# Kernel optimization log

Hardware: AMD Instinct MI355X
Metric: run time of the kernel (lower is better)

## Reference

```python
import jax, jax.numpy as jnp
import numpy as np

N = 100_000   # nodes
E = 1_600_000 # edges (avg degree 16)
IN_DIM = 128
OUT_DIM = 64
NEG_SLOPE = 0.2  # PyG GATConv default


def setup_inputs() -> dict:
    key = jax.random.key(0)
    k_x, k_ei, k_w, k_as, k_ad = jax.random.split(key, 5)
    x = jax.random.normal(k_x, (N, IN_DIM), dtype=jnp.float32)
    edge_index = jax.random.randint(k_ei, (2, E), 0, N, dtype=jnp.int32)
    # GATConv params (heads=1): linear weight, attention vectors, output bias
    W = jax.random.normal(k_w, (IN_DIM, OUT_DIM), dtype=jnp.float32) / np.sqrt(IN_DIM)
    a_src = jax.random.normal(k_as, (OUT_DIM,), dtype=jnp.float32) * 0.1
    a_dst = jax.random.normal(k_ad, (OUT_DIM,), dtype=jnp.float32) * 0.1
    bias = jnp.zeros((OUT_DIM,), dtype=jnp.float32)
    return {"x": x, "edge_index": edge_index, "W": W, "a_src": a_src, "a_dst": a_dst, "bias": bias}


def reference(x, edge_index, W, a_src, a_dst, bias):
    # PyG GATConv, heads=1, add_self_loops=True
    h = x @ W                                   # [N, OUT]
    loop = jnp.arange(N, dtype=edge_index.dtype)
    ei = jnp.concatenate([edge_index, jnp.stack([loop, loop])], axis=1)  # [2, E+N]
    src, dst = ei[0], ei[1]
    # per-node attention logits, gathered per edge
    alpha_s = h @ a_src                         # [N]
    alpha_d = h @ a_dst                         # [N]
    e = alpha_s[src] + alpha_d[dst]             # [E+N]
    e = jnp.where(e > 0, e, NEG_SLOPE * e)      # leaky_relu
    # segment softmax over edges sharing the same destination node
    m = jax.ops.segment_max(e, dst, num_segments=N)   # every node has a self loop
    ex = jnp.exp(e - m[dst])
    s = jax.ops.segment_sum(ex, dst, num_segments=N)
    alpha = ex / s[dst]                         # [E+N]
    # weighted scatter-add of source messages
    out = jax.ops.segment_sum(alpha[:, None] * h[src], dst, num_segments=N)  # [N, OUT]
    return out + bias
```

## Files before the change

### kernel.cpp

```cpp
#include <hip/hip_runtime.h>
#include <hip/hip_bf16.h>

#ifndef NEG_SLOPE
#define NEG_SLOPE 0.2f
#endif

#define GRP_SHIFT 9
#define GRP_SIZE 512
#define NGMAX 256
#define MS_CHUNK 4096
#define BKT_CAP 10240

typedef short bf16x8 __attribute__((ext_vector_type(8)));
typedef float f32x4 __attribute__((ext_vector_type(4)));

__device__ __forceinline__ unsigned short f2bf(float f) {
    union { float f; unsigned int u; } c; c.f = f;
    unsigned int r = (c.u + 0x7FFFu + ((c.u >> 16) & 1u)) >> 16;
    return (unsigned short)r;
}
__device__ __forceinline__ float bf2f(unsigned short u) {
    union { unsigned int u; float f; } c; c.u = ((unsigned int)u) << 16;
    return c.f;
}
__device__ __forceinline__ float bflo(unsigned int u) {
    union { unsigned int u; float f; } c; c.u = u << 16;
    return c.f;
}
__device__ __forceinline__ float bfhi(unsigned int u) {
    union { unsigned int u; float f; } c; c.u = u & 0xffff0000u;
    return c.f;
}

struct GemmSmem {
    unsigned short xb[64 * 136];
    unsigned short wt[64 * 136];
};
struct MsSmem {
    unsigned int pack[MS_CHUNK];
    unsigned char gtag[MS_CHUNK];
    int hist[NGMAX];
    int gb[NGMAX];
    int wsum[4];
};
union FusedSmem {
    GemmSmem g;
    MsSmem m;
};

__global__ __launch_bounds__(256) void gemm_ms_kernel(
    const float* __restrict__ x, const float* __restrict__ W,
    const float* __restrict__ a_src, const float* __restrict__ a_dst,
    unsigned short* __restrict__ hb, float* __restrict__ as_,
    float* __restrict__ ad_, const int* __restrict__ ei,
    int* __restrict__ cursor, unsigned int* __restrict__ pairs,
    int N, int E, int NG, int nchunk)
{
    __shared__ FusedSmem sm;
    const int tid = threadIdx.x;

    if ((int)blockIdx.x < nchunk) {
        unsigned int* ls_pack = sm.m.pack;
        unsigned char* ls_g = sm.m.gtag;
        int* ls_hist = sm.m.hist;
        int* ls_gb = sm.m.gb;
        int* ls_wsum = sm.m.wsum;

        const int cs = (int)blockIdx.x * MS_CHUNK;
        const int n = min(MS_CHUNK, E - cs);
        const int* srcp = ei + cs;
        const int* dstp = ei + E + cs;

        ls_hist[tid] = 0;
        __syncthreads();
        for (int i = tid; i < n; i += 256)
            atomicAdd(&ls_hist[dstp[i] >> GRP_SHIFT], 1);
        __syncthreads();

        const int h = ls_hist[tid];
        const int lane = tid & 63;
        int incl = h;
#pragma unroll
        for (int off = 1; off < 64; off <<= 1) {
            const int t = __shfl_up(incl, off);
            if (lane >= off) incl += t;
        }
        const int wv = tid >> 6;
        if (lane == 63) ls_wsum[wv] = incl;
        __syncthreads();
        int wpre = 0;
        for (int w = 0; w < wv; ++w) wpre += ls_wsum[w];
        const int excl = wpre + incl - h;
        if (tid < NG && h > 0) {
            const int old = atomicAdd(&cursor[tid], h);
            ls_gb[tid] = tid * BKT_CAP + old - excl;
        }
        __syncthreads();
        ls_hist[tid] = excl;
        __syncthreads();

        for (int i = tid; i < n; i += 256) {
            const int src = srcp[i];
            const int dst = dstp[i];
            const int g = dst >> GRP_SHIFT;
            const int idx = atomicAdd(&ls_hist[g], 1);
            ls_pack[idx] = ((unsigned int)src << GRP_SHIFT) | (unsigned int)(dst & (GRP_SIZE - 1));
            ls_g[idx] = (unsigned char)g;
        }
        __syncthreads();

        for (int i = tid; i < n; i += 256) {
            const int g = ls_g[i];
            const int pos = ls_gb[g] + i;
            if (pos < (g + 1) * BKT_CAP)
                pairs[pos] = ls_pack[i];
        }
    } else {
        unsigned short* xb = sm.g.xb;
        unsigned short* wt = sm.g.wt;
        const int r0 = ((int)blockIdx.x - nchunk) * 64;

        for (int idx = tid; idx < 2048; idx += 256) {
            const int r = idx >> 5;
            const int c4 = idx & 31;
            const int row = r0 + r;
            float4 v = make_float4(0.f, 0.f, 0.f, 0.f);
            if (row < N) v = ((const float4*)(x + (size_t)row * 128))[c4];
            ushort4 o;
            o.x = f2bf(v.x); o.y = f2bf(v.y); o.z = f2bf(v.z); o.w = f2bf(v.w);
            *(ushort4*)(xb + r * 136 + c4 * 4) = o;
        }
        {
            const int n = tid & 63;
            const int kb = (tid >> 6) * 32;
            for (int kk = 0; kk < 32; ++kk) {
                const int k = kb + kk;
                wt[n * 136 + k] = f2bf(W[k * 64 + n]);
            }
        }
        __syncthreads();

        const int wv = tid >> 6;
        const int lane = tid & 63;
        const int m16 = lane & 15;
        const int quad = lane >> 4;

        f32x4 acc[4];
#pragma unroll
        for (int ct = 0; ct < 4; ++ct) acc[ct] = (f32x4){0.f, 0.f, 0.f, 0.f};

        const unsigned short* xrow = xb + (wv * 16 + m16) * 136;
#pragma unroll
        for (int kq = 0; kq < 4; ++kq) {
            const int k0 = kq * 32;
            const bf16x8 a = *(const bf16x8*)(xrow + k0 + quad * 8);
#pragma unroll
            for (int ct = 0; ct < 4; ++ct) {
                const bf16x8 b = *(const bf16x8*)(wt + (ct * 16 + m16) * 136 + k0 + quad * 8);
                acc[ct] = __builtin_amdgcn_mfma_f32_16x16x32_bf16(a, b, acc[ct], 0, 0, 0);
            }
        }

#pragma unroll
        for (int ct = 0; ct < 4; ++ct) {
#pragma unroll
            for (int rg = 0; rg < 4; ++rg) {
                const int row = r0 + wv * 16 + quad * 4 + rg;
                if (row < N) hb[(size_t)row * 64 + ct * 16 + m16] = f2bf(acc[ct][rg]);
            }
        }

        float asv[4], adv[4];
#pragma unroll
        for (int ct = 0; ct < 4; ++ct) {
            asv[ct] = a_src[ct * 16 + m16];
            adv[ct] = a_dst[ct * 16 + m16];
        }
#pragma unroll
        for (int rg = 0; rg < 4; ++rg) {
            float ps = acc[0][rg] * asv[0] + acc[1][rg] * asv[1] +
                       acc[2][rg] * asv[2] + acc[3][rg] * asv[3];
            float pd = acc[0][rg] * adv[0] + acc[1][rg] * adv[1] +
                       acc[2][rg] * adv[2] + acc[3][rg] * adv[3];
#pragma unroll
            for (int off = 1; off < 16; off <<= 1) {
                ps += __shfl_xor(ps, off);
                pd += __shfl_xor(pd, off);
            }
            const int row = r0 + wv * 16 + quad * 4 + rg;
            if (m16 == 0 && row < N) { as_[row] = ps; ad_[row] = pd; }
        }
    }
}

__global__ __launch_bounds__(1024) void group_sort_kernel(
    const unsigned int* __restrict__ pairs, const int* __restrict__ cursor,
    unsigned int* __restrict__ meta, int* __restrict__ csr, int N)
{
    __shared__ int sdeg[GRP_SIZE];
    __shared__ int scur[GRP_SIZE];
    __shared__ int swsum[8];
    __shared__ int ssrc[BKT_CAP];
    const int g = blockIdx.x;
    const int tid = threadIdx.x;
    const int eb0 = g * BKT_CAP;
    const int cnt = min(cursor[g], BKT_CAP);

    if (tid < GRP_SIZE) sdeg[tid] = 0;
    __syncthreads();
    for (int i = tid; i < cnt; i += 1024)
        atomicAdd(&sdeg[pairs[eb0 + i] & (GRP_SIZE - 1)], 1);
    __syncthreads();

    int s = 0, incl = 0;
    if (tid < GRP_SIZE) {
        s = sdeg[tid];
        const int lane = tid & 63;
        incl = s;
#pragma unroll
        for (int off = 1; off < 64; off <<= 1) {
            const int t = __shfl_up(incl, off);
            if (lane >= off) incl += t;
        }
        if (lane == 63) swsum[tid >> 6] = incl;
    }
    __syncthreads();
    if (tid < GRP_SIZE) {
        int wpre = 0;
        const int wv = tid >> 6;
        for (int w = 0; w < wv; ++w) wpre += swsum[w];
        const int excl = wpre + incl - s;
        scur[tid] = excl;
        const int node = (g << GRP_SHIFT) + tid;
        if (node < N)
            meta[node] = ((unsigned int)(eb0 + excl) << 10) | (unsigned int)min(s, 1023);
    }
    __syncthreads();

    for (int i = tid; i < cnt; i += 1024) {
        const unsigned int p = pairs[eb0 + i];
        const int idx = atomicAdd(&scur[p & (GRP_SIZE - 1)], 1);
        ssrc[idx] = (int)(p >> GRP_SHIFT);
    }
    __syncthreads();
    for (int i = tid; i < cnt; i += 1024)
        csr[eb0 + i] = ssrc[i];
}

__device__ void aggregate_slow(
    const unsigned short* __restrict__ h, const float* __restrict__ as_,
    const float* __restrict__ ad_, const int* __restrict__ csr,
    const float* __restrict__ bias, float* __restrict__ out,
    int wid, int p0, int deg, int lane)
{
    const float adi = ad_[wid];
    float e0 = as_[wid] + adi;
    e0 = e0 > 0.f ? e0 : NEG_SLOPE * e0;
    float m = e0, ll = 1.f;
    float acc = bf2f(h[(size_t)wid * 64 + lane]);
    const int p1 = p0 + deg;
    for (int p = p0; p < p1; ++p) {
        const int sj = csr[p];
        float ee = as_[sj] + adi;
        ee = ee > 0.f ? ee : NEG_SLOPE * ee;
        const float nm = fmaxf(m, ee);
        const float sc = __expf(m - nm);
        const float pp = __expf(ee - nm);
        ll = ll * sc + pp;
        acc = acc * sc + pp * bf2f(h[(size_t)sj * 64 + lane]);
        m = nm;
    }
    out[(size_t)wid * 64 + lane] = acc / ll + bias[lane];
}

__global__ __launch_bounds__(256) void aggregate_kernel(
    const unsigned short* __restrict__ h, const float* __restrict__ as_,
    const float* __restrict__ ad_, const unsigned int* __restrict__ meta,
    const int* __restrict__ csr, const float* __restrict__ bias,
    float* __restrict__ out, int N)
{
    const int wbase = (blockIdx.x * 256 + threadIdx.x) >> 6;
    const int lane = threadIdx.x & 63;
    const int widA = wbase * 2;
    if (widA >= N) return;
    const int widB = widA + 1;
    const bool hasB = (widB < N);

    const unsigned int mtA = meta[widA];
    const unsigned int mtB = hasB ? meta[widB] : 0u;
    const int p0A = (int)(mtA >> 10), degA = (int)(mtA & 1023u);
    const int p0B = (int)(mtB >> 10), degB = (int)(mtB & 1023u);

    if (degA <= 63 && degB <= 63) {
        const float adiA = ad_[widA];
        const float adiB = hasB ? ad_[widB] : 0.f;
        float e0A = as_[widA] + adiA;
        e0A = e0A > 0.f ? e0A : NEG_SLOPE * e0A;
        float e0B = hasB ? as_[widB] + adiB : 0.f;
        e0B = e0B > 0.f ? e0B : NEG_SLOPE * e0B;

        int sA = widA, sB = hasB ? widB : widA;
        float eA = -1e30f, eB = -1e30f;
        if (lane < degA) {
            sA = csr[p0A + lane];
            const float t = as_[sA] + adiA;
            eA = t > 0.f ? t : NEG_SLOPE * t;
        } else if (lane == degA) {
            eA = e0A;
        }
        if (hasB) {
            if (lane < degB) {
                sB = csr[p0B + lane];
                const float t = as_[sB] + adiB;
                eB = t > 0.f ? t : NEG_SLOPE * t;
            } else if (lane == degB) {
                eB = e0B;
            }
        }

        float mA = eA, mB = eB;
#pragma unroll
        for (int off = 1; off < 64; off <<= 1) {
            mA = fmaxf(mA, __shfl_xor(mA, off));
            mB = fmaxf(mB, __shfl_xor(mB, off));
        }
        const float peA = __expf(eA - mA);
        const float peB = hasB ? __expf(eB - mB) : 0.f;
        float lA = peA, lB = peB;
#pragma unroll
        for (int off = 1; off < 64; off <<= 1) {
            lA += __shfl_xor(lA, off);
            lB += __shfl_xor(lB, off);
        }

        const int half = lane >> 5;
        const int l5 = lane & 31;
        const unsigned int* hb32 = (const unsigned int*)h;
        float a0 = 0.f, a1 = 0.f, b0 = 0.f, b1 = 0.f;
        const int npA = (degA + 2) >> 1;
        const int npB = hasB ? (degB + 2) >> 1 : 0;
        const int npMax = max(npA, npB);

        for (int jp = 0; jp < npMax; jp += 4) {
            const int sl0 = (jp    ) * 2 + half;
            const int sl1 = (jp + 1) * 2 + half;
            const int sl2 = (jp + 2) * 2 + half;
            const int sl3 = (jp + 3) * 2 + half;
            const int sa0 = __shfl(sA, sl0), sa1 = __shfl(sA, sl1);
            const int sa2 = __shfl(sA, sl2), sa3 = __shfl(sA, sl3);
            const int sb0 = __shfl(sB, sl0), sb1 = __shfl(sB, sl1);
            const int sb2 = __shfl(sB, sl2), sb3 = __shfl(sB, sl3);
            const float wa0 = __shfl(peA, sl0), wa1 = __shfl(peA, sl1);
            const float wa2 = __shfl(peA, sl2), wa3 = __shfl(peA, sl3);
            const float wb0 = __shfl(peB, sl0), wb1 = __shfl(peB, sl1);
            const float wb2 = __shfl(peB, sl2), wb3 = __shfl(peB, sl3);
            const unsigned int ua0 = hb32[sa0 * 32 + l5];
            const unsigned int ua1 = hb32[sa1 * 32 + l5];
            const unsigned int ua2 = hb32[sa2 * 32 + l5];
            const unsigned int ua3 = hb32[sa3 * 32 + l5];
            const unsigned int ub0 = hb32[sb0 * 32 + l5];
            const unsigned int ub1 = hb32[sb1 * 32 + l5];
            const unsigned int ub2 = hb32[sb2 * 32 + l5];
            const unsigned int ub3 = hb32[sb3 * 32 + l5];
            a0 += wa0 * bflo(ua0); a1 += wa0 * bfhi(ua0);
            a0 += wa1 * bflo(ua1); a1 += wa1 * bfhi(ua1);
            a0 += wa2 * bflo(ua2); a1 += wa2 * bfhi(ua2);
            a0 += wa3 * bflo(ua3); a1 += wa3 * bfhi(ua3);
            b0 += wb0 * bflo(ub0); b1 += wb0 * bfhi(ub0);
            b0 += wb1 * bflo(ub1); b1 += wb1 * bfhi(ub1);
            b0 += wb2 * bflo(ub2); b1 += wb2 * bfhi(ub2);
            b0 += wb3 * bflo(ub3); b1 += wb3 * bfhi(ub3);
        }
        a0 += __shfl_xor(a0, 32);
        a1 += __shfl_xor(a1, 32);
        b0 += __shfl_xor(b0, 32);
        b1 += __shfl_xor(b1, 32);
        if (half == 0) {
            const float2 bv = ((const float2*)bias)[l5];
            float2 oA;
            oA.x = a0 / lA + bv.x;
            oA.y = a1 / lA + bv.y;
            ((float2*)(out + (size_t)widA * 64))[l5] = oA;
            if (hasB) {
                float2 oB;
                oB.x = b0 / lB + bv.x;
                oB.y = b1 / lB + bv.y;
                ((float2*)(out + (size_t)widB * 64))[l5] = oB;
            }
        }
    } else {
        aggregate_slow(h, as_, ad_, csr, bias, out, widA, p0A, degA, lane);
        if (hasB) aggregate_slow(h, as_, ad_, csr, bias, out, widB, p0B, degB, lane);
    }
}

extern "C" void kernel_launch(void* const* d_in, const int* in_sizes, int n_in,
                              void* d_out, int out_size, void* d_ws, size_t ws_size,
                              hipStream_t stream)
{
    const float* x     = (const float*)d_in[0];
    const int*   ei    = (const int*)d_in[1];
    const float* W     = (const float*)d_in[2];
    const float* a_src = (const float*)d_in[3];
    const float* a_dst = (const float*)d_in[4];
    const float* bias  = (const float*)d_in[5];
    float* out = (float*)d_out;

    const int N = in_sizes[0] / 128;
    const int E = in_sizes[1] / 2;
    const int NG = (N + GRP_SIZE - 1) >> GRP_SHIFT;
    const int nchunk = (E + MS_CHUNK - 1) / MS_CHUNK;
    const int gemmBlocks = (N + 63) / 64;

    unsigned short* hb = (unsigned short*)d_ws;
    float* alpha_s = (float*)(hb + (size_t)N * 64);
    float* alpha_d = alpha_s + N;
    int* cursor = (int*)(alpha_d + N);
    unsigned int* meta = (unsigned int*)(cursor + NG);
    int* csr = (int*)(meta + N);
    unsigned int* pairs = (unsigned int*)(csr + (size_t)NG * BKT_CAP);

    hipMemsetAsync(cursor, 0, (size_t)NG * sizeof(int), stream);
    gemm_ms_kernel<<<nchunk + gemmBlocks, 256, 0, stream>>>(
        x, W, a_src, a_dst, hb, alpha_s, alpha_d, ei, cursor, pairs,
        N, E, NG, nchunk);
    group_sort_kernel<<<NG, 1024, 0, stream>>>(pairs, cursor, meta, csr, N);
    aggregate_kernel<<<(N + 7) / 8, 256, 0, stream>>>(hb, alpha_s, alpha_d, meta,
                                                      csr, bias, out, N);
}
```

Before: 176.4 us.

## Shrink destination groups to 128 nodes and widen aggregate gathers to 8 bytes

```diff
diff --git a/kernel.cpp b/kernel.cpp
--- a/kernel.cpp
+++ b/kernel.cpp
@@ -5,11 +5,11 @@
 #define NEG_SLOPE 0.2f
 #endif
 
-#define GRP_SHIFT 9
-#define GRP_SIZE 512
-#define NGMAX 256
+#define GRP_SHIFT 7
+#define GRP_SIZE 128
+#define NBINS 1024
 #define MS_CHUNK 4096
-#define BKT_CAP 10240
+#define BKT_CAP 2560
 
 typedef short bf16x8 __attribute__((ext_vector_type(8)));
 typedef float f32x4 __attribute__((ext_vector_type(4)));
@@ -38,9 +38,9 @@
 };
 struct MsSmem {
     unsigned int pack[MS_CHUNK];
-    unsigned char gtag[MS_CHUNK];
-    int hist[NGMAX];
-    int gb[NGMAX];
+    unsigned short gtag[MS_CHUNK];
+    int hist[NBINS];
+    int gb[NBINS];
     int wsum[4];
 };
 union FusedSmem {
@@ -61,7 +61,7 @@
 
     if ((int)blockIdx.x < nchunk) {
         unsigned int* ls_pack = sm.m.pack;
-        unsigned char* ls_g = sm.m.gtag;
+        unsigned short* ls_g = sm.m.gtag;
         int* ls_hist = sm.m.hist;
         int* ls_gb = sm.m.gb;
         int* ls_wsum = sm.m.wsum;
@@ -71,15 +71,18 @@
         const int* srcp = ei + cs;
         const int* dstp = ei + E + cs;
 
-        ls_hist[tid] = 0;
+        for (int i = tid; i < NBINS; i += 256) ls_hist[i] = 0;
         __syncthreads();
         for (int i = tid; i < n; i += 256)
             atomicAdd(&ls_hist[dstp[i] >> GRP_SHIFT], 1);
         __syncthreads();
 
-        const int h = ls_hist[tid];
+        const int b0 = tid * 4;
+        const int h0 = ls_hist[b0], h1 = ls_hist[b0 + 1];
+        const int h2 = ls_hist[b0 + 2], h3 = ls_hist[b0 + 3];
+        const int s = h0 + h1 + h2 + h3;
         const int lane = tid & 63;
-        int incl = h;
+        int incl = s;
 #pragma unroll
         for (int off = 1; off < 64; off <<= 1) {
             const int t = __shfl_up(incl, off);
@@ -90,13 +93,22 @@
         __syncthreads();
         int wpre = 0;
         for (int w = 0; w < wv; ++w) wpre += ls_wsum[w];
-        const int excl = wpre + incl - h;
-        if (tid < NG && h > 0) {
-            const int old = atomicAdd(&cursor[tid], h);
-            ls_gb[tid] = tid * BKT_CAP + old - excl;
-        }
-        __syncthreads();
-        ls_hist[tid] = excl;
+        int ex = wpre + incl - s;
+        const int hh[4] = {h0, h1, h2, h3};
+        int exs[4];
+#pragma unroll
+        for (int j = 0; j < 4; ++j) { exs[j] = ex; ex += hh[j]; }
+#pragma unroll
+        for (int j = 0; j < 4; ++j) {
+            const int g = b0 + j;
+            if (g < NG && hh[j] > 0) {
+                const int old = atomicAdd(&cursor[g], hh[j]);
+                ls_gb[g] = g * BKT_CAP + old - exs[j];
+            }
+        }
+        __syncthreads();
+#pragma unroll
+        for (int j = 0; j < 4; ++j) ls_hist[b0 + j] = exs[j];
         __syncthreads();
 
         for (int i = tid; i < n; i += 256) {
@@ -105,7 +117,7 @@
             const int g = dst >> GRP_SHIFT;
             const int idx = atomicAdd(&ls_hist[g], 1);
             ls_pack[idx] = ((unsigned int)src << GRP_SHIFT) | (unsigned int)(dst & (GRP_SIZE - 1));
-            ls_g[idx] = (unsigned char)g;
+            ls_g[idx] = (unsigned short)g;
         }
         __syncthreads();
 
@@ -193,13 +205,13 @@
     }
 }
 
-__global__ __launch_bounds__(1024) void group_sort_kernel(
+__global__ __launch_bounds__(256) void group_sort_kernel(
     const unsigned int* __restrict__ pairs, const int* __restrict__ cursor,
     unsigned int* __restrict__ meta, int* __restrict__ csr, int N)
 {
     __shared__ int sdeg[GRP_SIZE];
     __shared__ int scur[GRP_SIZE];
-    __shared__ int swsum[8];
+    __shared__ int swsum[2];
     __shared__ int ssrc[BKT_CAP];
     const int g = blockIdx.x;
     const int tid = threadIdx.x;
@@ -208,7 +220,7 @@
 
     if (tid < GRP_SIZE) sdeg[tid] = 0;
     __syncthreads();
-    for (int i = tid; i < cnt; i += 1024)
+    for (int i = tid; i < cnt; i += 256)
         atomicAdd(&sdeg[pairs[eb0 + i] & (GRP_SIZE - 1)], 1);
     __syncthreads();
 
@@ -226,9 +238,7 @@
     }
     __syncthreads();
     if (tid < GRP_SIZE) {
-        int wpre = 0;
-        const int wv = tid >> 6;
-        for (int w = 0; w < wv; ++w) wpre += swsum[w];
+        const int wpre = (tid >= 64) ? swsum[0] : 0;
         const int excl = wpre + incl - s;
         scur[tid] = excl;
         const int node = (g << GRP_SHIFT) + tid;
@@ -237,13 +247,13 @@
     }
     __syncthreads();
 
-    for (int i = tid; i < cnt; i += 1024) {
+    for (int i = tid; i < cnt; i += 256) {
         const unsigned int p = pairs[eb0 + i];
         const int idx = atomicAdd(&scur[p & (GRP_SIZE - 1)], 1);
         ssrc[idx] = (int)(p >> GRP_SHIFT);
     }
     __syncthreads();
-    for (int i = tid; i < cnt; i += 1024)
+    for (int i = tid; i < cnt; i += 256)
         csr[eb0 + i] = ssrc[i];
 }
 
@@ -333,19 +343,20 @@
             lB += __shfl_xor(lB, off);
         }
 
-        const int half = lane >> 5;
-        const int l5 = lane & 31;
-        const unsigned int* hb32 = (const unsigned int*)h;
-        float a0 = 0.f, a1 = 0.f, b0 = 0.f, b1 = 0.f;
-        const int npA = (degA + 2) >> 1;
-        const int npB = hasB ? (degB + 2) >> 1 : 0;
-        const int npMax = max(npA, npB);
-
-        for (int jp = 0; jp < npMax; jp += 4) {
-            const int sl0 = (jp    ) * 2 + half;
-            const int sl1 = (jp + 1) * 2 + half;
-            const int sl2 = (jp + 2) * 2 + half;
-            const int sl3 = (jp + 3) * 2 + half;
+        const int q = lane >> 4;
+        const int l4 = lane & 15;
+        const uint2* hq = (const uint2*)h;
+        float a0 = 0.f, a1 = 0.f, a2 = 0.f, a3 = 0.f;
+        float b0 = 0.f, b1 = 0.f, b2 = 0.f, b3 = 0.f;
+        const int nqA = (degA + 4) >> 2;
+        const int nqB = hasB ? (degB + 4) >> 2 : 0;
+        const int nqMax = max(nqA, nqB);
+
+        for (int t = 0; t < nqMax; t += 4) {
+            const int sl0 = (t    ) * 4 + q;
+            const int sl1 = (t + 1) * 4 + q;
+            const int sl2 = (t + 2) * 4 + q;
+            const int sl3 = (t + 3) * 4 + q;
             const int sa0 = __shfl(sA, sl0), sa1 = __shfl(sA, sl1);
             const int sa2 = __shfl(sA, sl2), sa3 = __shfl(sA, sl3);
             const int sb0 = __shfl(sB, sl0), sb1 = __shfl(sB, sl1);
@@ -354,38 +365,51 @@
             const float wa2 = __shfl(peA, sl2), wa3 = __shfl(peA, sl3);
             const float wb0 = __shfl(peB, sl0), wb1 = __shfl(peB, sl1);
             const float wb2 = __shfl(peB, sl2), wb3 = __shfl(peB, sl3);
-            const unsigned int ua0 = hb32[sa0 * 32 + l5];
-            const unsigned int ua1 = hb32[sa1 * 32 + l5];
-            const unsigned int ua2 = hb32[sa2 * 32 + l5];
-            const unsigned int ua3 = hb32[sa3 * 32 + l5];
-            const unsigned int ub0 = hb32[sb0 * 32 + l5];
-            const unsigned int ub1 = hb32[sb1 * 32 + l5];
-            const unsigned int ub2 = hb32[sb2 * 32 + l5];
-            const unsigned int ub3 = hb32[sb3 * 32 + l5];
-            a0 += wa0 * bflo(ua0); a1 += wa0 * bfhi(ua0);
-            a0 += wa1 * bflo(ua1); a1 += wa1 * bfhi(ua1);
-            a0 += wa2 * bflo(ua2); a1 += wa2 * bfhi(ua2);
-            a0 += wa3 * bflo(ua3); a1 += wa3 * bfhi(ua3);
-            b0 += wb0 * bflo(ub0); b1 += wb0 * bfhi(ub0);
-            b0 += wb1 * bflo(ub1); b1 += wb1 * bfhi(ub1);
-            b0 += wb2 * bflo(ub2); b1 += wb2 * bfhi(ub2);
-            b0 += wb3 * bflo(ub3); b1 += wb3 * bfhi(ub3);
-        }
-        a0 += __shfl_xor(a0, 32);
-        a1 += __shfl_xor(a1, 32);
-        b0 += __shfl_xor(b0, 32);
-        b1 += __shfl_xor(b1, 32);
-        if (half == 0) {
-            const float2 bv = ((const float2*)bias)[l5];
-            float2 oA;
-            oA.x = a0 / lA + bv.x;
-            oA.y = a1 / lA + bv.y;
-            ((float2*)(out + (size_t)widA * 64))[l5] = oA;
+            const uint2 ua0 = hq[sa0 * 16 + l4];
+            const uint2 ua1 = hq[sa1 * 16 + l4];
+            const uint2 ua2 = hq[sa2 * 16 + l4];
+            const uint2 ua3 = hq[sa3 * 16 + l4];
+            const uint2 ub0 = hq[sb0 * 16 + l4];
+            const uint2 ub1 = hq[sb1 * 16 + l4];
+            const uint2 ub2 = hq[sb2 * 16 + l4];
+            const uint2 ub3 = hq[sb3 * 16 + l4];
+            a0 += wa0 * bflo(ua0.x); a1 += wa0 * bfhi(ua0.x);
+            a2 += wa0 * bflo(ua0.y); a3 += wa0 * bfhi(ua0.y);
+            a0 += wa1 * bflo(ua1.x); a1 += wa1 * bfhi(ua1.x);
+            a2 += wa1 * bflo(ua1.y); a3 += wa1 * bfhi(ua1.y);
+            a0 += wa2 * bflo(ua2.x); a1 += wa2 * bfhi(ua2.x);
+            a2 += wa2 * bflo(ua2.y); a3 += wa2 * bfhi(ua2.y);
+            a0 += wa3 * bflo(ua3.x); a1 += wa3 * bfhi(ua3.x);
+            a2 += wa3 * bflo(ua3.y); a3 += wa3 * bfhi(ua3.y);
+            b0 += wb0 * bflo(ub0.x); b1 += wb0 * bfhi(ub0.x);
+            b2 += wb0 * bflo(ub0.y); b3 += wb0 * bfhi(ub0.y);
+            b0 += wb1 * bflo(ub1.x); b1 += wb1 * bfhi(ub1.x);
+            b2 += wb1 * bflo(ub1.y); b3 += wb1 * bfhi(ub1.y);
+            b0 += wb2 * bflo(ub2.x); b1 += wb2 * bfhi(ub2.x);
+            b2 += wb2 * bflo(ub2.y); b3 += wb2 * bfhi(ub2.y);
+            b0 += wb3 * bflo(ub3.x); b1 += wb3 * bfhi(ub3.x);
+            b2 += wb3 * bflo(ub3.y); b3 += wb3 * bfhi(ub3.y);
+        }
+#pragma unroll
+        for (int off = 16; off <= 32; off <<= 1) {
+            a0 += __shfl_xor(a0, off); a1 += __shfl_xor(a1, off);
+            a2 += __shfl_xor(a2, off); a3 += __shfl_xor(a3, off);
+            b0 += __shfl_xor(b0, off); b1 += __shfl_xor(b1, off);
+            b2 += __shfl_xor(b2, off); b3 += __shfl_xor(b3, off);
+        }
+        if (q == 0) {
+            const float4 bv = ((const float4*)bias)[l4];
+            const float rA = 1.f / lA;
+            float4 oA;
+            oA.x = a0 * rA + bv.x; oA.y = a1 * rA + bv.y;
+            oA.z = a2 * rA + bv.z; oA.w = a3 * rA + bv.w;
+            ((float4*)(out + (size_t)widA * 64))[l4] = oA;
             if (hasB) {
-                float2 oB;
-                oB.x = b0 / lB + bv.x;
-                oB.y = b1 / lB + bv.y;
-                ((float2*)(out + (size_t)widB * 64))[l5] = oB;
+                const float rB = 1.f / lB;
+                float4 oB;
+                oB.x = b0 * rB + bv.x; oB.y = b1 * rB + bv.y;
+                oB.z = b2 * rB + bv.z; oB.w = b3 * rB + bv.w;
+                ((float4*)(out + (size_t)widB * 64))[l4] = oB;
             }
         }
     } else {
@@ -424,7 +448,7 @@
     gemm_ms_kernel<<<nchunk + gemmBlocks, 256, 0, stream>>>(
         x, W, a_src, a_dst, hb, alpha_s, alpha_d, ei, cursor, pairs,
         N, E, NG, nchunk);
-    group_sort_kernel<<<NG, 1024, 0, stream>>>(pairs, cursor, meta, csr, N);
+    group_sort_kernel<<<NG, 256, 0, stream>>>(pairs, cursor, meta, csr, N);
     aggregate_kernel<<<(N + 7) / 8, 256, 0, stream>>>(hb, alpha_s, alpha_d, meta,
                                                       csr, bias, out, N);
 }
```

Measured after the change: 207.9 us. 17.9% more time.
